# Optimization experiments

Measured on AMD Instinct MI355X. Metric: run time of the kernel, lower is better.

Reference implementation:

```python
import jax, jax.numpy as jnp
import numpy as np

IN_FEATURES = 512
DIM_EXPLOSION = 20
OUT_FEATURES = IN_FEATURES * DIM_EXPLOSION  # 10240
NB_PROJ_ENTRIES = 6
HASH_LENGTH = 32
BATCH = 4096


def _make_sparse_proj(key):
    """Sparse binary random projection: each of the OUT_FEATURES rows has
    NB_PROJ_ENTRIES entries set to 1 (as in OlfactoryModel.create_rand_proj_matrix)."""
    idx = jax.random.randint(key, (OUT_FEATURES, NB_PROJ_ENTRIES), 0, IN_FEATURES)
    rows = jnp.arange(OUT_FEATURES)[:, None]
    W = jnp.zeros((OUT_FEATURES, IN_FEATURES), dtype=jnp.float32)
    return W.at[rows, idx].set(1.0)


def setup_inputs() -> dict:
    key = jax.random.key(0)
    k1, k2 = jax.random.split(key)
    inp = jax.random.uniform(k1, (BATCH, IN_FEATURES), dtype=jnp.float32)
    W = _make_sparse_proj(k2)
    return {"input": inp, "weight": W, "hash_length": HASH_LENGTH}


def reference(input, weight, hash_length):
    # F.linear: [B, in] @ [out, in]^T -> [B, out]
    x = jnp.einsum('bi,oi->bo', input, weight)
    # MB_sparsify: winner-take-all, keep top `hash_length` activations per row, zero the rest
    topv = jax.lax.top_k(x, hash_length)[0]          # [B, k]
    thresh = topv[:, -1:]                            # k-th largest per row
    return jnp.where(x >= thresh, x, jnp.zeros_like(x))
```

## Files before the change

### kernel.cpp

```cpp
#include <hip/hip_runtime.h>


typedef float f4 __attribute__((ext_vector_type(4)));

constexpr int IN_F   = 512;
constexpr int OUT_F  = 10240;
constexpr int TPB    = 1024;
constexpr int ROWS   = 4;
constexpr int FPT    = OUT_F / TPB;
constexpr int NBINS  = 1024;
constexpr int NWAVES = TPB / 64;
constexpr int CAP    = 64;

static_assert(NBINS == 64 * 16, "wave scan assumes 16 bins per lane");

__global__ __launch_bounds__(256) void extract_idx(const float* __restrict__ W,
                                                   uint4* __restrict__ packed,
                                                   int out_f) {
  int row  = blockIdx.x * 4 + (threadIdx.x >> 6);
  int lane = threadIdx.x & 63;
  if (row >= out_f) return;

  const float* wr = W + (size_t)row * IN_F;
  unsigned long long masks[8];
#pragma unroll
  for (int c = 0; c < 8; ++c) {
    float v = wr[c * 64 + lane];
    masks[c] = __ballot(v != 0.0f);
  }
  if (lane == 0) {
    unsigned idx[6] = {IN_F, IN_F, IN_F, IN_F, IN_F, IN_F};
    int n = 0;
#pragma unroll
    for (int c = 0; c < 8; ++c) {
      unsigned long long m = masks[c];
      while (m && n < 6) {
        int b = __builtin_ctzll(m);
        idx[n++] = (unsigned)(c * 64 + b);
        m &= m - 1;
      }
    }
    uint4 r;
    r.x = idx[0] | (idx[1] << 16);
    r.y = idx[2] | (idx[3] << 16);
    r.z = idx[4] | (idx[5] << 16);
    r.w = (unsigned)n;
    packed[row] = r;
  }
}

__device__ __forceinline__ float row_val(const f4* in4, uint4 p, int r) {
  const float* b = (const float*)in4;
  float s = b[(p.x & 0xFFFFu) * 4 + r];
  s += b[(p.x >> 16) * 4 + r];
  s += b[(p.y & 0xFFFFu) * 4 + r];
  s += b[(p.y >> 16) * 4 + r];
  s += b[(p.z & 0xFFFFu) * 4 + r];
  s += b[(p.z >> 16) * 4 + r];
  return s;
}

__global__ __launch_bounds__(TPB, 4) void fly_hash(const float* __restrict__ inp,
                                                   const uint4* __restrict__ packed,
                                                   const int* __restrict__ kptr,
                                                   float* __restrict__ out) {
  __shared__ f4    in4[IN_F + 1];
  __shared__ int   hist[ROWS * NBINS];
  __shared__ int   wsum[NWAVES];
  __shared__ int   sh_bstar[ROWS], sh_above[ROWS], sh_n[ROWS], sh_cnt[ROWS];
  __shared__ float sh_list[ROWS][CAP];
  __shared__ float sh_thr[ROWS];
  __shared__ int   sh_need[ROWS];

  const int tid  = threadIdx.x;
  const int lane = tid & 63;
  const int wid  = tid >> 6;
  const int row0 = blockIdx.x * ROWS;
  const int k    = *kptr;

  if (tid < IN_F) {
    const float* p = inp + (size_t)row0 * IN_F + tid;
    f4 v;
    v.x = p[0];
    v.y = p[IN_F];
    v.z = p[2 * IN_F];
    v.w = p[3 * IN_F];
    in4[tid] = v;
  } else if (tid == IN_F) {
    f4 z = {0.0f, 0.0f, 0.0f, 0.0f};
    in4[IN_F] = z;
  }
  if (tid < ROWS) { sh_bstar[tid] = -1; sh_cnt[tid] = 0; }
  for (int i = tid; i < ROWS * NBINS; i += TPB) hist[i] = 0;
  __syncthreads();

  uint4 rk[FPT];
#pragma unroll
  for (int i = 0; i < FPT; ++i) rk[i] = packed[tid + i * TPB];

  f4 x4[FPT];
#pragma unroll
  for (int i = 0; i < FPT; ++i) {
    uint4 r = rk[i];
    f4 s = in4[r.x & 0xFFFFu];
    s += in4[r.x >> 16];
    s += in4[r.y & 0xFFFFu];
    s += in4[r.y >> 16];
    s += in4[r.z & 0xFFFFu];
    s += in4[r.z >> 16];
    x4[i] = s;
#pragma unroll
    for (int rr = 0; rr < ROWS; ++rr) {
      float v = s[rr];
      if (v >= 4.0f) {
        int b = (int)((v - 4.0f) * 512.0f);
        b = b > NBINS - 1 ? NBINS - 1 : b;
        atomicAdd(&hist[rr * NBINS + b], 1);
      }
    }
  }
  __syncthreads();

  if (wid < ROWS) {
    const int r = wid;
    const int base = r * NBINS + lane * 16;
    int csum = 0;
#pragma unroll
    for (int j = 0; j < 16; ++j) csum += hist[base + j];
    int s = csum;
#pragma unroll
    for (int off = 1; off < 64; off <<= 1) {
      int t = __shfl_down(s, off);
      if (lane + off < 64) s += t;
    }
    int s_next = __shfl_down(s, 1);
    if (lane == 63) s_next = 0;
    if (s >= k && s_next < k) {
      int acc = s_next;
      int bsel = lane * 16, abv = s_next;
      for (int b = lane * 16 + 15; b >= lane * 16; --b) {
        int h = hist[r * NBINS + b];
        if (acc + h >= k) { bsel = b; abv = acc; break; }
        acc += h;
      }
      sh_bstar[r] = bsel;
      sh_above[r] = abv;
      sh_n[r]     = hist[r * NBINS + bsel];
    }
  }
  __syncthreads();

  {
    const int b0 = sh_bstar[0], b1 = sh_bstar[1];
    const int b2 = sh_bstar[2], b3 = sh_bstar[3];
#pragma unroll
    for (int i = 0; i < FPT; ++i) {
      f4 s = x4[i];
#pragma unroll
      for (int rr = 0; rr < ROWS; ++rr) {
        float v = s[rr];
        int bb = (rr == 0) ? b0 : (rr == 1) ? b1 : (rr == 2) ? b2 : b3;
        if (v >= 4.0f) {
          int b = (int)((v - 4.0f) * 512.0f);
          b = b > NBINS - 1 ? NBINS - 1 : b;
          if (b == bb) {
            int p = atomicAdd(&sh_cnt[rr], 1);
            if (p < CAP) sh_list[rr][p] = v;
          }
        }
      }
    }
  }
  __syncthreads();

  if (wid < ROWS) {
    const int r   = wid;
    const int bst = sh_bstar[r];
    const int n   = (bst >= 0) ? sh_n[r] : CAP + 1;
    if (bst >= 0 && n <= CAP && sh_cnt[r] <= CAP) {
      const int j = k - sh_above[r];
      float vl = (lane < n) ? sh_list[r][lane] : -1.0f;
      int cgt = 0, cge = 0;
      for (int m = 0; m < n; ++m) {
        float u = sh_list[r][m];
        cgt += (u > vl);
        cge += (u >= vl);
      }
      if (lane < n && cgt < j && cge >= j) sh_thr[r] = vl;
      if (lane == 0) sh_need[r] = 0;
    } else {
      if (lane == 0) sh_need[r] = 1;
    }
  }
  __syncthreads();

#pragma unroll 1
  for (int r = 0; r < ROWS; ++r) {
    if (!sh_need[r]) continue;
    unsigned lo = 0u, hi = __float_as_uint(8.0f);
    while (lo < hi) {
      unsigned mid = lo + ((hi - lo + 1u) >> 1);
      float fm = __uint_as_float(mid);
      int c = 0;
      for (int i = 0; i < FPT; ++i) {
        uint4 p = packed[tid + i * TPB];
        c += (int)__popcll(__ballot(row_val(in4, p, r) >= fm));
      }
      if (lane == 0) wsum[wid] = c;
      __syncthreads();
      int tot = 0;
#pragma unroll
      for (int w = 0; w < NWAVES; ++w) tot += wsum[w];
      if (tot >= k) lo = mid; else hi = mid - 1u;
      __syncthreads();
    }
    if (tid == 0) sh_thr[r] = __uint_as_float(lo);
    __syncthreads();
  }
  const float t0 = sh_thr[0];
  const float t1 = sh_thr[1];
  const float t2 = sh_thr[2];
  const float t3 = sh_thr[3];

  float* o0 = out + (size_t)(row0 + 0) * OUT_F;
  float* o1 = out + (size_t)(row0 + 1) * OUT_F;
  float* o2 = out + (size_t)(row0 + 2) * OUT_F;
  float* o3 = out + (size_t)(row0 + 3) * OUT_F;
#pragma unroll
  for (int i = 0; i < FPT; ++i) {
    int f = tid + i * TPB;
    f4 v = x4[i];
    __builtin_nontemporal_store((v.x >= t0) ? v.x : 0.0f, &o0[f]);
    __builtin_nontemporal_store((v.y >= t1) ? v.y : 0.0f, &o1[f]);
    __builtin_nontemporal_store((v.z >= t2) ? v.z : 0.0f, &o2[f]);
    __builtin_nontemporal_store((v.w >= t3) ? v.w : 0.0f, &o3[f]);
  }
}

extern "C" void kernel_launch(void* const* d_in, const int* in_sizes, int n_in,
                              void* d_out, int out_size, void* d_ws, size_t ws_size,
                              hipStream_t stream) {
  const float* inp = (const float*)d_in[0];
  const float* W   = (const float*)d_in[1];
  const int* kptr  = (const int*)d_in[2];
  float* out       = (float*)d_out;

  const int batch = in_sizes[0] / IN_F;
  const int out_f = in_sizes[1] / IN_F;

  uint4* packed = (uint4*)d_ws;

  hipLaunchKernelGGL(extract_idx, dim3((out_f + 3) / 4), dim3(256), 0, stream,
                     W, packed, out_f);
  hipLaunchKernelGGL(fly_hash, dim3(batch / ROWS), dim3(TPB), 0, stream,
                     inp, packed, kptr, out);
}
```

Baseline: 244.2 us.

## Zero-fill output early to overlap stores with compute, then scatter winners

Each block now writes zeros to its whole output tile at the start, before the top-k selection, so the bulk store traffic overlaps the histogram and threshold phases. At the end only the surviving activations are written, after waiting on outstanding memory ops. The packed index loads are hoisted ahead of the shared-memory setup. Barriers are replaced by an LDS-only wait plus s_barrier so they no longer drain pending global stores. This relies on the zero stores being ordered before the sparse overwrites, and the vmcnt wait could stall the block.

Measured after the change: 276.1 us. 13.1% more time.

```diff
diff --git a/kernel.cpp b/kernel.cpp
--- a/kernel.cpp
+++ b/kernel.cpp
@@ -13,6 +13,11 @@
 constexpr int CAP    = 64;
 
 static_assert(NBINS == 64 * 16, "wave scan assumes 16 bins per lane");
+
+__device__ __forceinline__ void bar_lds() {
+  asm volatile("s_waitcnt lgkmcnt(0)" ::: "memory");
+  __builtin_amdgcn_s_barrier();
+}
 
 __global__ __launch_bounds__(256) void extract_idx(const float* __restrict__ W,
                                                    uint4* __restrict__ packed,
@@ -78,25 +83,42 @@
   const int row0 = blockIdx.x * ROWS;
   const int k    = *kptr;
 
+  float* o0 = out + (size_t)(row0 + 0) * OUT_F;
+  float* o1 = out + (size_t)(row0 + 1) * OUT_F;
+  float* o2 = out + (size_t)(row0 + 2) * OUT_F;
+  float* o3 = out + (size_t)(row0 + 3) * OUT_F;
+
+  uint4 rk[FPT];
+#pragma unroll
+  for (int i = 0; i < FPT; ++i) rk[i] = packed[tid + i * TPB];
+
+  f4 sv = {0.0f, 0.0f, 0.0f, 0.0f};
   if (tid < IN_F) {
     const float* p = inp + (size_t)row0 * IN_F + tid;
-    f4 v;
-    v.x = p[0];
-    v.y = p[IN_F];
-    v.z = p[2 * IN_F];
-    v.w = p[3 * IN_F];
-    in4[tid] = v;
+    sv.x = p[0];
+    sv.y = p[IN_F];
+    sv.z = p[2 * IN_F];
+    sv.w = p[3 * IN_F];
+  }
+
+#pragma unroll
+  for (int i = 0; i < FPT; ++i) {
+    int f = tid + i * TPB;
+    __builtin_nontemporal_store(0.0f, &o0[f]);
+    __builtin_nontemporal_store(0.0f, &o1[f]);
+    __builtin_nontemporal_store(0.0f, &o2[f]);
+    __builtin_nontemporal_store(0.0f, &o3[f]);
+  }
+
+  if (tid < IN_F) {
+    in4[tid] = sv;
   } else if (tid == IN_F) {
     f4 z = {0.0f, 0.0f, 0.0f, 0.0f};
     in4[IN_F] = z;
   }
   if (tid < ROWS) { sh_bstar[tid] = -1; sh_cnt[tid] = 0; }
   for (int i = tid; i < ROWS * NBINS; i += TPB) hist[i] = 0;
-  __syncthreads();
-
-  uint4 rk[FPT];
-#pragma unroll
-  for (int i = 0; i < FPT; ++i) rk[i] = packed[tid + i * TPB];
+  bar_lds();
 
   f4 x4[FPT];
 #pragma unroll
@@ -119,7 +141,7 @@
       }
     }
   }
-  __syncthreads();
+  bar_lds();
 
   if (wid < ROWS) {
     const int r = wid;
@@ -148,7 +170,7 @@
       sh_n[r]     = hist[r * NBINS + bsel];
     }
   }
-  __syncthreads();
+  bar_lds();
 
   {
     const int b0 = sh_bstar[0], b1 = sh_bstar[1];
@@ -171,7 +193,7 @@
       }
     }
   }
-  __syncthreads();
+  bar_lds();
 
   if (wid < ROWS) {
     const int r   = wid;
@@ -192,7 +214,7 @@
       if (lane == 0) sh_need[r] = 1;
     }
   }
-  __syncthreads();
+  bar_lds();
 
 #pragma unroll 1
   for (int r = 0; r < ROWS; ++r) {
@@ -222,18 +244,15 @@
   const float t2 = sh_thr[2];
   const float t3 = sh_thr[3];
 
-  float* o0 = out + (size_t)(row0 + 0) * OUT_F;
-  float* o1 = out + (size_t)(row0 + 1) * OUT_F;
-  float* o2 = out + (size_t)(row0 + 2) * OUT_F;
-  float* o3 = out + (size_t)(row0 + 3) * OUT_F;
+  asm volatile("s_waitcnt vmcnt(0)" ::: "memory");
 #pragma unroll
   for (int i = 0; i < FPT; ++i) {
     int f = tid + i * TPB;
     f4 v = x4[i];
-    __builtin_nontemporal_store((v.x >= t0) ? v.x : 0.0f, &o0[f]);
-    __builtin_nontemporal_store((v.y >= t1) ? v.y : 0.0f, &o1[f]);
-    __builtin_nontemporal_store((v.z >= t2) ? v.z : 0.0f, &o2[f]);
-    __builtin_nontemporal_store((v.w >= t3) ? v.w : 0.0f, &o3[f]);
+    if (v.x >= t0) o0[f] = v.x;
+    if (v.y >= t1) o1[f] = v.y;
+    if (v.z >= t2) o2[f] = v.z;
+    if (v.w >= t3) o3[f] = v.w;
   }
 }
 
```
